# Performance work log

Measured on AMD Instinct MI355X. Metric: run time of the kernel, lower is better.

The kernel has to match this reference:

```python
import jax, jax.numpy as jnp
import numpy as np
jax.config.update("jax_enable_x64", True)  # hash uses int64 like torch .long()

N_LEVELS = 16
F = 16
B = 1.38
BASE_RES = 16
T_PRIME = 1048583  # nextprime(2**20)
PS = np.array([1, 19349663, 83492791], dtype=np.int64)
BBOX = np.array([[-2., -2., -2.], [2., 2., 2.]], dtype=np.float32)
ENTRIES_NUM = np.array([int(BASE_RES * B ** i) for i in range(N_LEVELS)], dtype=np.int64)
ENTRIES_CNT = ENTRIES_NUM ** 3
ENTRIES_SIZE = (1.0 / (ENTRIES_NUM - 1)).astype(np.float32)
ENTRIES_SUM = np.cumsum(ENTRIES_CNT)
START_HASH = int(np.argmax(ENTRIES_CNT > T_PRIME))  # = 6
DENSE_TOTAL = int(ENTRIES_SUM[START_HASH - 1])      # = 822944
OFFSETS = np.array([[0,0,0],[0,0,1],[0,1,0],[0,1,1],[1,0,0],[1,0,1],[1,1,0],[1,1,1]], dtype=np.float32)

def setup_inputs() -> dict:
    key = jax.random.key(0)
    k1, k2, k3 = jax.random.split(key, 3)
    N = 65536
    xyz = jax.random.uniform(k1, (N, 3), dtype=jnp.float32, minval=-2.0, maxval=2.0)
    # kaiming_normal_ on a (L, T, F) tensor: fan_in = T*F, gain = sqrt(2)
    std = float(np.sqrt(2.0 / (T_PRIME * F)))
    dense = jax.random.normal(k2, (DENSE_TOTAL, F), dtype=jnp.float32) * std
    hash_table = jax.random.normal(k3, (N_LEVELS - START_HASH, T_PRIME, F), dtype=jnp.float32) * std
    return {"xyz": xyz, "dense": dense, "hash_table": hash_table}

def reference(xyz, dense, hash_table):
    bash = xyz.shape
    x = xyz.reshape(-1, 3)
    lo = jnp.asarray(BBOX[0]); hi = jnp.asarray(BBOX[1])
    xn = (x - lo) / (hi - lo)                                  # [N,3] in [0,1]
    es = jnp.asarray(ENTRIES_SIZE)                             # [L]
    num = jnp.asarray(ENTRIES_NUM)                             # [L] int64
    offs = jnp.asarray(OFFSETS)                                # [8,3]
    flt = xn[None] / es[:, None, None]                         # [L,N,3]
    int_xyz = (flt[:, :, None] + offs[None, None]).astype(jnp.int64)  # [L,N,8,3]
    int_xyz = jnp.clip(int_xyz, 0, (num - 1)[:, None, None, None])
    off = flt - int_xyz[:, :, 0].astype(flt.dtype)             # [L,N,3]
    S = START_HASH; H = N_LEVELS - S
    nS = num[:S][:, None, None]
    ind_dense = int_xyz[:S, ..., 0] * nS * nS + int_xyz[:S, ..., 1] * nS + int_xyz[:S, ..., 2]
    dense_off = jnp.concatenate([jnp.zeros((1,), jnp.int64), jnp.asarray(ENTRIES_SUM[:S - 1])])
    ind_dense = ind_dense + dense_off[:, None, None]           # [S,N,8]
    ih = int_xyz[S:]
    ind_hash = ((ih[..., 0] * PS[0]) ^ (ih[..., 1] * PS[1]) ^ (ih[..., 2] * PS[2])) % T_PRIME  # [H,N,8]
    val_dense = dense[ind_dense]                               # [S,N,8,F]
    val_hash = hash_table[jnp.arange(H)[:, None, None], ind_hash]  # [H,N,8,F]
    val = jnp.concatenate([val_dense, val_hash], axis=0)       # [L,N,8,F]
    mul = 1.0 - offs[None, None] + (2.0 * offs[None, None] - 1.0) * off[:, :, None]  # [L,N,8,3]
    w = mul[..., 0] * mul[..., 1]  # NOTE: original code omits the z weight; faithful
    val = (w[..., None] * val).sum(axis=-2)                    # [L,N,F]
    val = jnp.transpose(val, (1, 0, 2))                        # [N,L,F]
    val = val.sum(axis=-1)                                     # [N,L] sum_over_features
    out = jnp.concatenate([xn, val], axis=-1)                  # [N,3+L]
    return out.reshape(*bash[:-1], out.shape[-1])
```

## Files before the change

kernel.cpp:

```cpp
#include <hip/hip_runtime.h>


#define HE_T_PRIME 1048583ULL
typedef unsigned long long ull;

static __device__ __constant__ int c_num[16] = {
    16, 22, 30, 42, 58, 80, 110, 152, 210, 290, 400, 553, 763, 1053, 1453, 2005};
static __device__ __constant__ float c_es[16] = {
    (float)(1.0 / 15.0),   (float)(1.0 / 21.0),   (float)(1.0 / 29.0),
    (float)(1.0 / 41.0),   (float)(1.0 / 57.0),   (float)(1.0 / 79.0),
    (float)(1.0 / 109.0),  (float)(1.0 / 151.0),  (float)(1.0 / 209.0),
    (float)(1.0 / 289.0),  (float)(1.0 / 399.0),  (float)(1.0 / 552.0),
    (float)(1.0 / 762.0),  (float)(1.0 / 1052.0), (float)(1.0 / 1452.0),
    (float)(1.0 / 2004.0)};
static __device__ __constant__ int c_doff[6] = {0, 4096, 14744, 41744, 115832, 310944};

__global__ __launch_bounds__(256) void HashEncoding_721554506107_kernel(
    const float* __restrict__ xyz, const float* __restrict__ dense,
    const float* __restrict__ hasht, float* __restrict__ out, int npts) {
  const int l = blockIdx.y;
  const int p = blockIdx.x * 64 + (threadIdx.x >> 2);
  const int q = threadIdx.x & 3;
  if (p >= npts) return;

  const float px = xyz[3 * p + 0];
  const float py = xyz[3 * p + 1];
  const float pz = xyz[3 * p + 2];
  const float xn0 = (px + 2.0f) * 0.25f;
  const float xn1 = (py + 2.0f) * 0.25f;
  const float xn2 = (pz + 2.0f) * 0.25f;
  if (l == 0 && q < 3) out[19 * p + q] = (q == 0) ? xn0 : ((q == 1) ? xn1 : xn2);

  const int n = c_num[l];
  const float es = c_es[l];
  const float fx = xn0 / es;
  const float fy = xn1 / es;
  const float fz = xn2 / es;
  const int nm1 = n - 1;
  const int ix0 = min(max((int)fx, 0), nm1);
  const int iy0 = min(max((int)fy, 0), nm1);
  const int iz0 = min(max((int)fz, 0), nm1);
  const int ix1 = min(max((int)(fx + 1.0f), 0), nm1);
  const int iy1 = min(max((int)(fy + 1.0f), 0), nm1);
  const int iz1 = min(max((int)(fz + 1.0f), 0), nm1);

  const float ox = fx - (float)ix0;
  const float oy = fy - (float)iy0;
  float wxy[4];
  wxy[0] = (1.0f - ox) * (1.0f - oy);
  wxy[1] = (1.0f - ox) * oy;
  wxy[2] = ox * (1.0f - oy);
  wxy[3] = ox * oy;

  float acc = 0.0f;
  if (l < 6) {
    const int nn = n * n;
    const int base = c_doff[l];
    const int ixs[2] = {ix0 * nn, ix1 * nn};
    const int iys[2] = {iy0 * n, iy1 * n};
    const int izs[2] = {iz0, iz1};
#pragma unroll
    for (int c = 0; c < 8; ++c) {
      const int ind = base + ixs[c >> 2] + iys[(c >> 1) & 1] + izs[c & 1];
      const float4 v =
          *(const float4*)(dense + (size_t)ind * 16 + (size_t)(q * 4));
      acc = fmaf(wxy[c >> 1], (v.x + v.y) + (v.z + v.w), acc);
    }
  } else {
    const float* tab = hasht + (size_t)(l - 6) * (size_t)(HE_T_PRIME * 16ULL);
    const ull hx[2] = {(ull)ix0, (ull)ix1};
    const ull hy[2] = {(ull)iy0 * 19349663ULL, (ull)iy1 * 19349663ULL};
    const ull hz[2] = {(ull)iz0 * 83492791ULL, (ull)iz1 * 83492791ULL};
#pragma unroll
    for (int c = 0; c < 8; ++c) {
      const ull h = hx[c >> 2] ^ hy[(c >> 1) & 1] ^ hz[c & 1];
      const size_t ind = (size_t)(h % HE_T_PRIME);
      const float4 v = *(const float4*)(tab + ind * 16 + (size_t)(q * 4));
      acc = fmaf(wxy[c >> 1], (v.x + v.y) + (v.z + v.w), acc);
    }
  }

  acc += __shfl_xor(acc, 1);
  acc += __shfl_xor(acc, 2);
  if (q == 0) out[19 * p + 3 + l] = acc;
}

extern "C" void kernel_launch(void* const* d_in, const int* in_sizes, int n_in,
                              void* d_out, int out_size, void* d_ws,
                              size_t ws_size, hipStream_t stream) {
  const float* xyz = (const float*)d_in[0];
  const float* dense = (const float*)d_in[1];
  const float* hasht = (const float*)d_in[2];
  float* out = (float*)d_out;
  const int npts = in_sizes[0] / 3;
  dim3 grid((npts + 63) / 64, 16);
  HashEncoding_721554506107_kernel<<<grid, 256, 0, stream>>>(xyz, dense, hasht,
                                                             out, npts);
}
```

Before: 117.7 us.

## Replace 64-bit hash modulo with 32-bit reduction, nontemporal loads, hash-first level order

Computes the 64-bit spatial hash modulo the prime using 32-bit arithmetic: the high word is folded via 2^32 mod p and only a 32-bit modulo remains, avoiding expensive 64-bit division. Hash-table gathers use nontemporal loads to reduce cache pollution. Block scheduling is remapped so the costly hash levels launch before the dense levels. The folding relies on the hash value's high part staying small, which holds because the grid indices are bounded.

```diff
diff --git a/kernel.cpp b/kernel.cpp
--- a/kernel.cpp
+++ b/kernel.cpp
@@ -1,8 +1,9 @@
 #include <hip/hip_runtime.h>
 
 
-#define HE_T_PRIME 1048583ULL
-typedef unsigned long long ull;
+#define HE_T_PRIME 1048583u
+#define HE_R32 1019911u
+typedef float __attribute__((ext_vector_type(4))) f32x4;
 
 static __device__ __constant__ int c_num[16] = {
     16, 22, 30, 42, 58, 80, 110, 152, 210, 290, 400, 553, 763, 1053, 1453, 2005};
@@ -18,7 +19,8 @@
 __global__ __launch_bounds__(256) void HashEncoding_721554506107_kernel(
     const float* __restrict__ xyz, const float* __restrict__ dense,
     const float* __restrict__ hasht, float* __restrict__ out, int npts) {
-  const int l = blockIdx.y;
+  const int y = blockIdx.y;
+  const int l = (y < 10) ? (y + 6) : (y - 10);
   const int p = blockIdx.x * 64 + (threadIdx.x >> 2);
   const int q = threadIdx.x & 3;
   if (p >= npts) return;
@@ -53,29 +55,38 @@
   wxy[3] = ox * oy;
 
   float acc = 0.0f;
-  if (l < 6) {
-    const int nn = n * n;
-    const int base = c_doff[l];
-    const int ixs[2] = {ix0 * nn, ix1 * nn};
-    const int iys[2] = {iy0 * n, iy1 * n};
-    const int izs[2] = {iz0, iz1};
+  if (l >= 6) {
+    const float* tabq =
+        hasht + (size_t)(l - 6) * (size_t)(HE_T_PRIME * 16ull) + (size_t)(q * 4);
+    const unsigned yl[2] = {(unsigned)iy0 * 19349663u, (unsigned)iy1 * 19349663u};
+    const unsigned yh[2] = {__umulhi((unsigned)iy0, 19349663u),
+                            __umulhi((unsigned)iy1, 19349663u)};
+    const unsigned zl[2] = {(unsigned)iz0 * 83492791u, (unsigned)iz1 * 83492791u};
+    const unsigned zh[2] = {__umulhi((unsigned)iz0, 83492791u),
+                            __umulhi((unsigned)iz1, 83492791u)};
+    const unsigned xl[2] = {(unsigned)ix0, (unsigned)ix1};
 #pragma unroll
     for (int c = 0; c < 8; ++c) {
-      const int ind = base + ixs[c >> 2] + iys[(c >> 1) & 1] + izs[c & 1];
-      const float4 v =
-          *(const float4*)(dense + (size_t)ind * 16 + (size_t)(q * 4));
+      const unsigned lo = xl[c >> 2] ^ yl[(c >> 1) & 1] ^ zl[c & 1];
+      const unsigned hi = yh[(c >> 1) & 1] ^ zh[c & 1];
+      const unsigned t = hi * HE_R32;
+      unsigned s = lo + t;
+      if (s < lo) s += HE_R32;
+      const unsigned ind = s % HE_T_PRIME;
+      const f32x4 v = __builtin_nontemporal_load(
+          (const f32x4*)(tabq + (size_t)(ind * 16u)));
       acc = fmaf(wxy[c >> 1], (v.x + v.y) + (v.z + v.w), acc);
     }
   } else {
-    const float* tab = hasht + (size_t)(l - 6) * (size_t)(HE_T_PRIME * 16ULL);
-    const ull hx[2] = {(ull)ix0, (ull)ix1};
-    const ull hy[2] = {(ull)iy0 * 19349663ULL, (ull)iy1 * 19349663ULL};
-    const ull hz[2] = {(ull)iz0 * 83492791ULL, (ull)iz1 * 83492791ULL};
+    const float* tabq = dense + (size_t)(c_doff[l] * 16) + (size_t)(q * 4);
+    const unsigned nn = (unsigned)(n * n);
+    const unsigned ixs[2] = {(unsigned)ix0 * nn, (unsigned)ix1 * nn};
+    const unsigned iys[2] = {(unsigned)(iy0 * n), (unsigned)(iy1 * n)};
+    const unsigned izs[2] = {(unsigned)iz0, (unsigned)iz1};
 #pragma unroll
     for (int c = 0; c < 8; ++c) {
-      const ull h = hx[c >> 2] ^ hy[(c >> 1) & 1] ^ hz[c & 1];
-      const size_t ind = (size_t)(h % HE_T_PRIME);
-      const float4 v = *(const float4*)(tab + ind * 16 + (size_t)(q * 4));
+      const unsigned ind = ixs[c >> 2] + iys[(c >> 1) & 1] + izs[c & 1];
+      const f32x4 v = *(const f32x4*)(tabq + (size_t)(ind * 16u));
       acc = fmaf(wxy[c >> 1], (v.x + v.y) + (v.z + v.w), acc);
     }
   }
```

New measurement: 127.9 us. 1.09x slower.
